# Kernel tuning notes

Measured on AMD Instinct MI355X. Metric: run time of the kernel, lower is better.

The kernel has to match this reference:

```python
import jax, jax.numpy as jnp
import numpy as np

B, IN_UNITS, IN_CHANNELS, NUM_UNITS, UNIT_SIZE = 256, 8, 1152, 10, 16
NUM_ITERS = 3


def setup_inputs() -> dict:
    key = jax.random.key(0)
    k1, k2 = jax.random.split(key)
    x = jax.random.normal(k1, (B, IN_UNITS, IN_CHANNELS), dtype=jnp.float32)
    # W from nn.Parameter(torch.randn(1, in_channels, num_units, unit_size, in_units)); drop leading 1
    W = jax.random.normal(k2, (IN_CHANNELS, NUM_UNITS, UNIT_SIZE, IN_UNITS), dtype=jnp.float32)
    return {"x": x, "W": W}


def reference(x, W):
    # x: [B, in_units=i, in_channels=j]; original transposes to [B, j, i]
    # u_hat = W @ x : [B, j, n, u]
    batch = x.shape[0]
    u_hat = jnp.einsum('jnui,bij->bjnu', W, x)
    b = jnp.zeros((IN_CHANNELS, NUM_UNITS), dtype=x.dtype)  # b_ij [j, n]
    v = None
    for _ in range(NUM_ITERS):
        # legacy F.softmax on 4D [1,j,n,1] -> dim=1 = in_channels axis
        c = jax.nn.softmax(b, axis=0)  # [j, n]
        s = jnp.einsum('jn,bjnu->bnu', c, u_hat)  # s_j: [B, n, u]
        # squash over dim=2 of [B,1,n,u,1] == num_units axis (axis=1 here)
        mag_sq = jnp.sum(s * s, axis=1, keepdims=True)  # [B, 1, u]
        v = (mag_sq / (1.0 + mag_sq)) * (s / jnp.sqrt(mag_sq))  # [B, n, u]
        # agreement: mean over batch of <u_hat, v>
        b = b + jnp.einsum('bjnu,bnu->jn', u_hat, v) / batch
    return v[..., None]  # [B, num_units, unit_size, 1] == v_j.squeeze(1)
```

## Files before the change

### kernel.cpp

```cpp
#include <hip/hip_runtime.h>
#include <stdint.h>

#define B   256
#define IU  8
#define JC  1152
#define NN  10
#define UU  16
#define NU  160
#define JN  11520
#define WROW 1280
#define NP  9216
#define KB  72

typedef short bf16x8 __attribute__((ext_vector_type(8)));
typedef float f32x4  __attribute__((ext_vector_type(4)));

__device__ __forceinline__ short f2bf(float f) {
    union { float f; uint32_t u; } cv; cv.f = f;
    uint32_t u = cv.u;
    uint32_t r = u + 0x7fffu + ((u >> 16) & 1u);
    return (short)(r >> 16);
}
__device__ __forceinline__ float bf2f(short h) {
    union { uint32_t u; float f; } cv; cv.u = ((uint32_t)(unsigned short)h) << 16;
    return cv.f;
}
__device__ __forceinline__ uint32_t bfbits(float f) {
    union { float f; uint32_t u; } cv; cv.f = f;
    return (cv.u + 0x7fffu + ((cv.u >> 16) & 1u)) >> 16;
}
__device__ __forceinline__ uint32_t pk2(float a, float b) {
    return bfbits(a) | (bfbits(b) << 16);
}

__global__ void __launch_bounds__(256, 2)
k_gemm1(const float* __restrict__ xg, const float* __restrict__ wg,
        const float* __restrict__ cptr, float* __restrict__ s_part) {
    const int kb = blockIdx.x, mt = blockIdx.y;
    const int tid = threadIdx.x;
    const int wv = tid >> 6, lane = tid & 63;
    const int q = lane >> 4, l16 = lane & 15;
    const int b0 = mt * 32;
    const int jb0 = kb * 16;
    const int mfrag = wv >> 1;
    const int ntb = (wv & 1) * 5;

    __shared__ __align__(16) short As[8 * 32 * 8];
    __shared__ __align__(16) short Bs[8 * 160 * 8];

    f32x4 acc[5];
    #pragma unroll
    for (int nt = 0; nt < 5; ++nt) acc[nt] = (f32x4){0.f, 0.f, 0.f, 0.f};

    for (int jc = 0; jc < 2; ++jc) {
        const int j0 = jb0 + jc * 8;
        __syncthreads();
        #pragma unroll
        for (int p = 0; p < 2; ++p) {
            int idx = tid + 256 * p;
            int jq  = idx & 1;
            int row = idx >> 1;
            int bl = row >> 3, ii = row & 7;
            const float4 xv = *reinterpret_cast<const float4*>(
                &xg[(size_t)(b0 + bl) * NP + ii * JC + j0 + jq*4]);
            int jjb = jq * 4;
            As[((jjb+0)*32 + bl)*8 + ii] = f2bf(xv.x);
            As[((jjb+1)*32 + bl)*8 + ii] = f2bf(xv.y);
            As[((jjb+2)*32 + bl)*8 + ii] = f2bf(xv.z);
            As[((jjb+3)*32 + bl)*8 + ii] = f2bf(xv.w);
        }
        #pragma unroll
        for (int p = 0; p < 5; ++p) {
            int ridx = tid + 256 * p;
            int jj = ridx / 160;
            int nu = ridx - jj * 160;
            int j  = j0 + jj;
            const float4* wp = reinterpret_cast<const float4*>(
                &wg[(size_t)j * WROW + (size_t)nu * 8]);
            float4 f0 = wp[0], f1 = wp[1];
            float cc = cptr ? cptr[j * NN + (nu >> 4)] : (1.0f / (float)JC);
            uint4 d;
            d.x = pk2(f0.x * cc, f0.y * cc);
            d.y = pk2(f0.z * cc, f0.w * cc);
            d.z = pk2(f1.x * cc, f1.y * cc);
            d.w = pk2(f1.z * cc, f1.w * cc);
            *reinterpret_cast<uint4*>(&Bs[(size_t)ridx * 8]) = d;
        }
        __syncthreads();
        #pragma unroll
        for (int s = 0; s < 2; ++s) {
            int jj = s*4 + q;
            bf16x8 av = *reinterpret_cast<const bf16x8*>(
                &As[((jj*32 + mfrag*16 + l16) << 3)]);
            #pragma unroll
            for (int nt = 0; nt < 5; ++nt) {
                bf16x8 bv = *reinterpret_cast<const bf16x8*>(
                    &Bs[((jj*160 + (ntb + nt)*16 + l16) << 3)]);
                acc[nt] = __builtin_amdgcn_mfma_f32_16x16x32_bf16(av, bv, acc[nt], 0, 0, 0);
            }
        }
    }
    float* dst = s_part + (size_t)(kb*8 + mt) * 5120;
    #pragma unroll
    for (int nt = 0; nt < 5; ++nt)
        #pragma unroll
        for (int reg = 0; reg < 4; ++reg)
            dst[(mfrag*16 + q*4 + reg) * 160 + (ntb + nt)*16 + l16] = acc[nt][reg];
}

__global__ void __launch_bounds__(320, 2)
k_reduce_s(const float* __restrict__ s_part, float* __restrict__ vdst) {
    const int b = blockIdx.x, tid = threadIdx.x;
    const int t = tid % 160, kq = tid / 160;
    const int mt = b >> 5, bl = b & 31;
    const size_t off = (size_t)mt * 5120 + bl * 160 + t;

    float s = 0.f;
    for (int r = 0; r < 36; ++r)
        s += s_part[(size_t)(kq*36 + r) * 40960 + off];

    __shared__ float red[2][160];
    __shared__ float sv[NU];
    __shared__ float fb[UU];
    red[kq][t] = s;
    __syncthreads();
    if (tid < NU) sv[tid] = red[0][tid] + red[1][tid];
    __syncthreads();
    if (tid < UU) {
        float m = 0.f;
        #pragma unroll
        for (int n = 0; n < NN; ++n) { float z = sv[n*16 + tid]; m = fmaf(z, z, m); }
        fb[tid] = sqrtf(m) / (1.f + m);
    }
    __syncthreads();
    if (tid < NU)
        vdst[(size_t)b * NU + tid] = sv[tid] * fb[tid & 15];
}

__global__ void __launch_bounds__(256, 2)
k_vxg(const float* __restrict__ vg, const float* __restrict__ xg,
      float* __restrict__ G) {
    const int np0 = blockIdx.x * 64, m0 = blockIdx.y * 32;
    const int tid = threadIdx.x;
    const int wv = tid >> 6, lane = tid & 63;
    const int q = lane >> 4, l16 = lane & 15;

    __shared__ __align__(16) short Ash[8 * 32 * 8];
    __shared__ __align__(16) short Asl[8 * 32 * 8];
    __shared__ __align__(16) short Bsh[8 * 64 * 8];
    __shared__ __align__(16) short Bsl[8 * 64 * 8];

    f32x4 acc[2];
    acc[0] = (f32x4){0.f,0.f,0.f,0.f};
    acc[1] = (f32x4){0.f,0.f,0.f,0.f};

    for (int ks = 0; ks < 4; ++ks) {
        const int b0 = ks * 64;
        __syncthreads();
        #pragma unroll
        for (int p = 0; p < 8; ++p) {
            int idx = tid + 256 * p;
            int bb = idx >> 5, ml = idx & 31;
            float vv = vg[(size_t)(b0 + bb) * NU + m0 + ml];
            short hi = f2bf(vv);
            short lo = f2bf(vv - bf2f(hi));
            int a = ((bb >> 3) * 32 + ml) * 8 + (bb & 7);
            Ash[a] = hi; Asl[a] = lo;
        }
        #pragma unroll
        for (int p = 0; p < 16; ++p) {
            int idx = tid + 256 * p;
            int bb = idx >> 6, nl = idx & 63;
            float xv = xg[(size_t)(b0 + bb) * NP + np0 + nl];
            short hi = f2bf(xv);
            short lo = f2bf(xv - bf2f(hi));
            int a = ((bb >> 3) * 64 + nl) * 8 + (bb & 7);
            Bsh[a] = hi; Bsl[a] = lo;
        }
        __syncthreads();
        #pragma unroll
        for (int s = 0; s < 2; ++s) {
            int kc = s*4 + q;
            bf16x8 bh = *reinterpret_cast<const bf16x8*>(&Bsh[((kc*64 + wv*16 + l16) << 3)]);
            bf16x8 bl = *reinterpret_cast<const bf16x8*>(&Bsl[((kc*64 + wv*16 + l16) << 3)]);
            #pragma unroll
            for (int mtl = 0; mtl < 2; ++mtl) {
                bf16x8 ah = *reinterpret_cast<const bf16x8*>(&Ash[((kc*32 + mtl*16 + l16) << 3)]);
                bf16x8 al = *reinterpret_cast<const bf16x8*>(&Asl[((kc*32 + mtl*16 + l16) << 3)]);
                acc[mtl] = __builtin_amdgcn_mfma_f32_16x16x32_bf16(ah, bh, acc[mtl], 0, 0, 0);
                acc[mtl] = __builtin_amdgcn_mfma_f32_16x16x32_bf16(ah, bl, acc[mtl], 0, 0, 0);
                acc[mtl] = __builtin_amdgcn_mfma_f32_16x16x32_bf16(al, bh, acc[mtl], 0, 0, 0);
            }
        }
    }
    #pragma unroll
    for (int mtl = 0; mtl < 2; ++mtl)
        #pragma unroll
        for (int reg = 0; reg < 4; ++reg) {
            int m  = m0 + mtl*16 + q*4 + reg;
            G[(size_t)m * NP + np0 + wv*16 + l16] = acc[mtl][reg];
        }
}

__global__ void k_wg_db(const float* __restrict__ wg, const float* __restrict__ G,
                        float* __restrict__ db) {
    const int j0 = blockIdx.x * 64, n = blockIdx.y;
    const int tid = threadIdx.x;
    const int jl = tid & 63, up = tid >> 6;
    const int j = j0 + jl;

    const float4* wp = reinterpret_cast<const float4*>(
        wg + (size_t)j * WROW + n * 128 + up * 32);
    float acc = 0.f;
    #pragma unroll
    for (int q4 = 0; q4 < 4; ++q4) {
        int u = up*4 + q4;
        const float* gp = G + (size_t)(n*16 + u) * NP + j;
        float4 w0 = wp[q4*2], w1 = wp[q4*2 + 1];
        acc = fmaf(w0.x, gp[0*JC], acc);
        acc = fmaf(w0.y, gp[1*JC], acc);
        acc = fmaf(w0.z, gp[2*JC], acc);
        acc = fmaf(w0.w, gp[3*JC], acc);
        acc = fmaf(w1.x, gp[4*JC], acc);
        acc = fmaf(w1.y, gp[5*JC], acc);
        acc = fmaf(w1.z, gp[6*JC], acc);
        acc = fmaf(w1.w, gp[7*JC], acc);
    }
    __shared__ float red[4][64];
    red[up][jl] = acc;
    __syncthreads();
    if (tid < 64)
        db[(size_t)(j0 + tid) * NN + n] =
            red[0][tid] + red[1][tid] + red[2][tid] + red[3][tid];
}

__global__ void k_softmax_upd(float* __restrict__ blog, const float* __restrict__ db,
                              float* __restrict__ c, float scale0) {
    int n = blockIdx.x;
    int tid = threadIdx.x;
    float myv[5]; int cnt = 0;
    for (int j = tid; j < JC; j += 256) {
        float val = blog[j*NN + n] * scale0 + db[j*NN + n] * (1.f / (float)B);
        blog[j*NN + n] = val;
        myv[cnt++] = val;
    }
    __shared__ float red[256];
    float m = -1e30f;
    for (int k = 0; k < cnt; ++k) m = fmaxf(m, myv[k]);
    red[tid] = m; __syncthreads();
    for (int s = 128; s > 0; s >>= 1) {
        if (tid < s) red[tid] = fmaxf(red[tid], red[tid+s]);
        __syncthreads();
    }
    m = red[0]; __syncthreads();
    float sum = 0.f;
    for (int k = 0; k < cnt; ++k) sum += __expf(myv[k] - m);
    red[tid] = sum; __syncthreads();
    for (int s = 128; s > 0; s >>= 1) {
        if (tid < s) red[tid] += red[tid+s];
        __syncthreads();
    }
    float inv = 1.f / red[0];
    cnt = 0;
    for (int j = tid; j < JC; j += 256)
        c[j*NN + n] = __expf(myv[cnt++] - m) * inv;
}

extern "C" void kernel_launch(void* const* d_in, const int* in_sizes, int n_in,
                              void* d_out, int out_size, void* d_ws, size_t ws_size,
                              hipStream_t stream) {
    const float* x = (const float*)d_in[0];
    const float* w = (const float*)d_in[1];
    float* out = (float*)d_out;

    float* ws     = (float*)d_ws;
    float* blog   = ws;
    float* c      = blog + JN;
    float* db     = c + JN;
    float* v      = db + JN;
    float* s_part = v + (size_t)B*NU;
    float* G      = s_part + (size_t)KB * 40960;

    for (int t = 0; t < 3; ++t) {
        k_gemm1<<<dim3(KB, 8), 256, 0, stream>>>(x, w, (t == 0) ? nullptr : c, s_part);
        k_reduce_s<<<B, 320, 0, stream>>>(s_part, (t == 2) ? out : v);
        if (t < 2) {
            k_vxg<<<dim3(144, 5), 256, 0, stream>>>(v, x, G);
            k_wg_db<<<dim3(18, 10), 256, 0, stream>>>(w, G, db);
            k_softmax_upd<<<NN, 256, 0, stream>>>(blog, db, c, (t == 0) ? 0.f : 1.f);
        }
    }
}
```

Before: 152.0 us.

## Fuse softmax update into agreement kernel via atomic exp-sum and deferred normalization

```diff
diff --git a/kernel.cpp b/kernel.cpp
--- a/kernel.cpp
+++ b/kernel.cpp
@@ -35,7 +35,8 @@
 
 __global__ void __launch_bounds__(256, 2)
 k_gemm1(const float* __restrict__ xg, const float* __restrict__ wg,
-        const float* __restrict__ cptr, float* __restrict__ s_part) {
+        const float* __restrict__ eblog, const float* __restrict__ expsum,
+        float* __restrict__ s_part) {
     const int kb = blockIdx.x, mt = blockIdx.y;
     const int tid = threadIdx.x;
     const int wv = tid >> 6, lane = tid & 63;
@@ -47,6 +48,9 @@
 
     __shared__ __align__(16) short As[8 * 32 * 8];
     __shared__ __align__(16) short Bs[8 * 160 * 8];
+    __shared__ float inv_s[NN];
+
+    if (eblog && tid < NN) inv_s[tid] = 1.f / expsum[tid];
 
     f32x4 acc[5];
     #pragma unroll
@@ -78,7 +82,9 @@
             const float4* wp = reinterpret_cast<const float4*>(
                 &wg[(size_t)j * WROW + (size_t)nu * 8]);
             float4 f0 = wp[0], f1 = wp[1];
-            float cc = cptr ? cptr[j * NN + (nu >> 4)] : (1.0f / (float)JC);
+            int nn = nu >> 4;
+            float cc = eblog ? eblog[j * NN + nn] * inv_s[nn]
+                             : (1.0f / (float)JC);
             uint4 d;
             d.x = pk2(f0.x * cc, f0.y * cc);
             d.y = pk2(f0.z * cc, f0.w * cc);
@@ -139,11 +145,13 @@
 
 __global__ void __launch_bounds__(256, 2)
 k_vxg(const float* __restrict__ vg, const float* __restrict__ xg,
-      float* __restrict__ G) {
+      float* __restrict__ G, float* __restrict__ expsum) {
     const int np0 = blockIdx.x * 64, m0 = blockIdx.y * 32;
     const int tid = threadIdx.x;
     const int wv = tid >> 6, lane = tid & 63;
     const int q = lane >> 4, l16 = lane & 15;
+
+    if (blockIdx.x == 0 && blockIdx.y == 0 && tid < NN) expsum[tid] = 0.f;
 
     __shared__ __align__(16) short Ash[8 * 32 * 8];
     __shared__ __align__(16) short Asl[8 * 32 * 8];
@@ -203,7 +211,8 @@
 }
 
 __global__ void k_wg_db(const float* __restrict__ wg, const float* __restrict__ G,
-                        float* __restrict__ db) {
+                        float* __restrict__ blog, float* __restrict__ eblog,
+                        float* __restrict__ expsum, int t0) {
     const int j0 = blockIdx.x * 64, n = blockIdx.y;
     const int tid = threadIdx.x;
     const int jl = tid & 63, up = tid >> 6;
@@ -229,41 +238,20 @@
     __shared__ float red[4][64];
     red[up][jl] = acc;
     __syncthreads();
-    if (tid < 64)
-        db[(size_t)(j0 + tid) * NN + n] =
-            red[0][tid] + red[1][tid] + red[2][tid] + red[3][tid];
-}
-
-__global__ void k_softmax_upd(float* __restrict__ blog, const float* __restrict__ db,
-                              float* __restrict__ c, float scale0) {
-    int n = blockIdx.x;
-    int tid = threadIdx.x;
-    float myv[5]; int cnt = 0;
-    for (int j = tid; j < JC; j += 256) {
-        float val = blog[j*NN + n] * scale0 + db[j*NN + n] * (1.f / (float)B);
-        blog[j*NN + n] = val;
-        myv[cnt++] = val;
-    }
-    __shared__ float red[256];
-    float m = -1e30f;
-    for (int k = 0; k < cnt; ++k) m = fmaxf(m, myv[k]);
-    red[tid] = m; __syncthreads();
-    for (int s = 128; s > 0; s >>= 1) {
-        if (tid < s) red[tid] = fmaxf(red[tid], red[tid+s]);
-        __syncthreads();
-    }
-    m = red[0]; __syncthreads();
-    float sum = 0.f;
-    for (int k = 0; k < cnt; ++k) sum += __expf(myv[k] - m);
-    red[tid] = sum; __syncthreads();
-    for (int s = 128; s > 0; s >>= 1) {
-        if (tid < s) red[tid] += red[tid+s];
-        __syncthreads();
-    }
-    float inv = 1.f / red[0];
-    cnt = 0;
-    for (int j = tid; j < JC; j += 256)
-        c[j*NN + n] = __expf(myv[cnt++] - m) * inv;
+    if (tid < 64) {
+        int jj = j0 + tid;
+        float d = (red[0][tid] + red[1][tid] + red[2][tid] + red[3][tid])
+                  * (1.f / (float)B);
+        float nb = t0 ? d : (blog[jj*NN + n] + d);
+        blog[jj*NN + n] = nb;
+        float e = __expf(nb);
+        eblog[jj*NN + n] = e;
+        float s = e;
+        s += __shfl_xor(s, 1);  s += __shfl_xor(s, 2);
+        s += __shfl_xor(s, 4);  s += __shfl_xor(s, 8);
+        s += __shfl_xor(s, 16); s += __shfl_xor(s, 32);
+        if (tid == 0) atomicAdd(&expsum[n], s);
+    }
 }
 
 extern "C" void kernel_launch(void* const* d_in, const int* in_sizes, int n_in,
@@ -275,19 +263,20 @@
 
     float* ws     = (float*)d_ws;
     float* blog   = ws;
-    float* c      = blog + JN;
-    float* db     = c + JN;
-    float* v      = db + JN;
+    float* eblog  = blog + JN;
+    float* expsum = eblog + JN;
+    float* v      = expsum + 16;
     float* s_part = v + (size_t)B*NU;
     float* G      = s_part + (size_t)KB * 40960;
 
     for (int t = 0; t < 3; ++t) {
-        k_gemm1<<<dim3(KB, 8), 256, 0, stream>>>(x, w, (t == 0) ? nullptr : c, s_part);
+        k_gemm1<<<dim3(KB, 8), 256, 0, stream>>>(
+            x, w, (t == 0) ? nullptr : eblog, expsum, s_part);
         k_reduce_s<<<B, 320, 0, stream>>>(s_part, (t == 2) ? out : v);
         if (t < 2) {
-            k_vxg<<<dim3(144, 5), 256, 0, stream>>>(v, x, G);
-            k_wg_db<<<dim3(18, 10), 256, 0, stream>>>(w, G, db);
-            k_softmax_upd<<<NN, 256, 0, stream>>>(blog, db, c, (t == 0) ? 0.f : 1.f);
-        }
-    }
-}
+            k_vxg<<<dim3(144, 5), 256, 0, stream>>>(v, x, G, expsum);
+            k_wg_db<<<dim3(18, 10), 256, 0, stream>>>(w, G, blog, eblog, expsum,
+                                                      (t == 0) ? 1 : 0);
+        }
+    }
+}
```

After: 147.9 us. -2.7%, faster.
